# Optimization experiments

Measured on AMD Instinct MI355X. Metric: run time of the kernel, lower is better.

The kernel has to match this reference:

```python
import jax, jax.numpy as jnp
import numpy as np
from functools import partial

BATCH, SEQ = 2, 2048
D_MODEL, D_INNER, D_XB = 2048, 4096, 1024
HEADDIM, D_STATE = 64, 64
NHEADS = D_INNER // HEADDIM      # 64
NKV = D_XB // HEADDIM            # 16
REP = NHEADS // NKV              # 4
INTER = 8192
EPS = 1e-5
D_IN_PROJ = D_INNER + D_XB + D_XB + D_INNER + NHEADS  # z, x, B, C, dt


def setup_inputs() -> dict:
    key = jax.random.key(0)
    ks = jax.random.split(key, 8)
    g = lambda k, shape, s: (jax.random.normal(k, shape, jnp.float32) * s)
    return {
        "hidden_states": g(ks[0], (BATCH, SEQ, D_MODEL), 1.0),
        "ln_w": jnp.ones((D_MODEL,), jnp.float32),
        "ln_b": jnp.zeros((D_MODEL,), jnp.float32),
        "in_proj_w": g(ks[1], (D_IN_PROJ, D_MODEL), 0.02),
        "dt_bias": jax.random.uniform(ks[2], (NHEADS,), jnp.float32, -4.0, 0.0),
        "A_log": jnp.log(jnp.arange(1, NHEADS + 1, dtype=jnp.float32)),
        "Dp": jnp.ones((NHEADS,), jnp.float32),
        "norm_w": jnp.ones((D_INNER,), jnp.float32),
        "out_proj_w": g(ks[3], (D_MODEL, D_INNER), 0.02),
        "fc1_w": g(ks[4], (INTER, D_MODEL), 0.02),
        "fc1_b": jnp.zeros((INTER,), jnp.float32),
        "fc2_w": g(ks[5], (D_MODEL, INTER), 0.02),
        "fc2_b": jnp.zeros((D_MODEL,), jnp.float32),
    }


def _layernorm(x, w, b):
    mu = x.mean(-1, keepdims=True)
    var = ((x - mu) ** 2).mean(-1, keepdims=True)
    return (x - mu) * jax.lax.rsqrt(var + EPS) * w + b


def _ssd_scan(xh, dt, A, Bh, Ch):
    # xh: (b,l,h,p)  dt: (b,l,h)  A: (h,)  Bh,Ch: (b,l,h,n)
    dA = jnp.exp(dt * A)  # (b,l,h) discrete decay
    to_l = lambda t: jnp.moveaxis(t, 1, 0)  # time-major for scan

    def step(state, inp):
        dA_t, dt_t, x_t, B_t, C_t = inp
        state = state * dA_t[:, :, None, None] + jnp.einsum(
            "bh,bhp,bhn->bhpn", dt_t, x_t, B_t)
        y = jnp.einsum("bhpn,bhn->bhp", state, C_t)
        return state, y

    state0 = jnp.zeros((xh.shape[0], NHEADS, HEADDIM, D_STATE), xh.dtype)
    _, ys = jax.lax.scan(step, state0, (to_l(dA), to_l(dt), to_l(xh), to_l(Bh), to_l(Ch)))
    return jnp.moveaxis(ys, 0, 1)  # (b,l,h,p)


def reference(hidden_states, ln_w, ln_b, in_proj_w, dt_bias, A_log, Dp,
              norm_w, out_proj_w, fc1_w, fc1_b, fc2_w, fc2_b):
    residual = hidden_states
    h = _layernorm(hidden_states, ln_w, ln_b)

    # ---- Mamba2 branch ----
    zxbcdt = h @ in_proj_w.T  # (b,l,D_IN_PROJ)
    z, x, Bm, Cm, dt = jnp.split(
        zxbcdt, np.cumsum([D_INNER, D_XB, D_XB, D_INNER]).tolist(), axis=-1)
    b, l = h.shape[0], h.shape[1]
    dt = jax.nn.softplus(dt + dt_bias)               # (b,l,nheads)
    A = -jnp.exp(A_log)                              # (nheads,)
    # GQA-style repeat of x (values) and B (keys) from NKV to NHEADS groups
    xh = jnp.repeat(x.reshape(b, l, NKV, HEADDIM), REP, axis=2)   # (b,l,h,p)
    Bh = jnp.repeat(Bm.reshape(b, l, NKV, D_STATE), REP, axis=2)  # (b,l,h,n)
    Ch = Cm.reshape(b, l, NHEADS, D_STATE)                        # (b,l,h,n)

    y = _ssd_scan(xh, dt, A, Bh, Ch) + Dp[None, None, :, None] * xh
    yf = y.reshape(b, l, D_INNER)
    # gated RMSNorm (norm_before_gate=False): gate first, then rmsnorm
    yf = yf * jax.nn.silu(z)
    yf = yf * jax.lax.rsqrt((yf * yf).mean(-1, keepdims=True) + EPS) * norm_w
    mamba_out = yf @ out_proj_w.T

    # ---- Phi MLP branch (parallel, shares the layernormed input) ----
    mlp = jax.nn.gelu(h @ fc1_w.T + fc1_b, approximate=True) @ fc2_w.T + fc2_b

    # resid_dropout is identity in eval mode
    return mamba_out + mlp + residual
```

## Files before the change

kernel.cpp:

```cpp
#include <hip/hip_runtime.h>
#include <hip/hip_bf16.h>

#define BATCH 2
#define SEQ   2048
#define DMODEL 2048
#define DINNER 4096
#define DXB   1024
#define NHEADS 64
#define NKV   16
#define HEADDIM 64
#define DSTATE 64
#define INTER 8192
#define DINPROJ 10304
#define ROWS  (BATCH*SEQ)
#define NC    32
#define EPSV  1e-5f
#define TSTR  72

typedef short short8 __attribute__((ext_vector_type(8)));
typedef float f32x4 __attribute__((ext_vector_type(4)));

typedef const __attribute__((address_space(1))) unsigned int cg_u32;
typedef __attribute__((address_space(3))) unsigned int ls_u32;

static __device__ __forceinline__ void gll16(const void* g, void* l) {
    __builtin_amdgcn_global_load_lds((cg_u32*)g, (ls_u32*)l, 16, 0, 0);
}

static __device__ __forceinline__ unsigned short f2bf(float f) {
    unsigned int u = __float_as_uint(f);
    unsigned int r = (u + 0x7fffu + ((u >> 16) & 1u)) >> 16;
    return (unsigned short)r;
}
static __device__ __forceinline__ float bf2f(unsigned short h) {
    return __uint_as_float(((unsigned int)h) << 16);
}

__global__ __launch_bounds__(256) void conv4(const float* __restrict__ s0, unsigned short* __restrict__ d0, int n0,
                                             const float* __restrict__ s1, unsigned short* __restrict__ d1, int n1,
                                             const float* __restrict__ s2, unsigned short* __restrict__ d2, int n2,
                                             const float* __restrict__ s3, unsigned short* __restrict__ d3, int n3) {
    int gtid = blockIdx.x * 256 + threadIdx.x;
    int gstr = gridDim.x * 256;
    #define CSEG(S, D, N)                                         \
    for (int i = gtid; i < (N); i += gstr) {                      \
        float4 v = ((const float4*)(S))[i];                       \
        ushort4 o;                                                \
        o.x = f2bf(v.x); o.y = f2bf(v.y);                         \
        o.z = f2bf(v.z); o.w = f2bf(v.w);                         \
        ((ushort4*)(D))[i] = o;                                   \
    }
    CSEG(s0, d0, n0)
    CSEG(s1, d1, n1)
    CSEG(s2, d2, n2)
    CSEG(s3, d3, n3)
    #undef CSEG
}

__global__ __launch_bounds__(256) void ln_kernel(const float* __restrict__ x,
                                                 const float* __restrict__ w,
                                                 const float* __restrict__ b,
                                                 unsigned short* __restrict__ hout) {
    int row = blockIdx.x;
    int t = threadIdx.x;
    const float* xr = x + (size_t)row * DMODEL;
    float v[8];
    float4 v0 = *(const float4*)&xr[t * 8];
    float4 v1 = *(const float4*)&xr[t * 8 + 4];
    v[0]=v0.x; v[1]=v0.y; v[2]=v0.z; v[3]=v0.w; v[4]=v1.x; v[5]=v1.y; v[6]=v1.z; v[7]=v1.w;
    float s = 0.f, s2 = 0.f;
    #pragma unroll
    for (int i = 0; i < 8; ++i) { s += v[i]; s2 += v[i]*v[i]; }
    #pragma unroll
    for (int off = 1; off < 64; off <<= 1) { s += __shfl_xor(s, off); s2 += __shfl_xor(s2, off); }
    __shared__ float sa[4], sb[4];
    int lane = t & 63, wv = t >> 6;
    if (lane == 0) { sa[wv] = s; sb[wv] = s2; }
    __syncthreads();
    s = sa[0]+sa[1]+sa[2]+sa[3];
    s2 = sb[0]+sb[1]+sb[2]+sb[3];
    float mu = s / DMODEL;
    float var = s2 / DMODEL - mu * mu;
    float sc = rsqrtf(var + EPSV);
    unsigned short* ho = hout + (size_t)row * DMODEL + t * 8;
    #pragma unroll
    for (int i = 0; i < 8; ++i) {
        int d = t * 8 + i;
        ho[i] = f2bf((v[i] - mu) * sc * w[d] + b[d]);
    }
}

#define SLOTSZ 49152
template <int EPI>
__global__ __launch_bounds__(512, 2) void gemm_p(
    const unsigned short* __restrict__ A, const unsigned short* __restrict__ B,
    int M, int N, int K, int nby,
    float* __restrict__ outF, unsigned short* __restrict__ outH,
    const float* __restrict__ bias, const float* __restrict__ add1,
    const float* __restrict__ add2,
    const unsigned short* __restrict__ A2, const unsigned short* __restrict__ B2,
    int K1) {
    __shared__ __align__(16) char smem[3 * SLOTSZ];
    int t = threadIdx.x, lane = t & 63, w = t >> 6;
    int nwg = gridDim.x, cpx = nwg >> 3;
    int logical = (blockIdx.x & 7) * cpx + (blockIdx.x >> 3);
    int by = logical % nby, bx = logical / nby;
    int brow = by * 128, bcol = bx * 256;
    int wr = w >> 2, wc = w & 3;
    int wrb = wr * 64, wcb = wc * 64;

    int lr8 = lane >> 3;
    int lch = ((lane & 7) ^ lr8) << 3;
    const unsigned short* pa[2];
    #pragma unroll
    for (int j = 0; j < 2; ++j)
        pa[j] = A + (size_t)(brow + w * 16 + j * 8 + lr8) * K1 + lch;
    const unsigned short* pb[4];
    #pragma unroll
    for (int j = 0; j < 4; ++j) {
        int r = bcol + w * 32 + j * 8 + lr8;
        if (r > N - 1) r = N - 1;
        pb[j] = B + (size_t)r * K1 + lch;
    }
    auto stageA = [&](int slot, int j) {
        gll16(pa[j], smem + slot * SLOTSZ + (w * 16 + j * 8) * 128);
        pa[j] += 64;
    };
    auto stageB = [&](int slot, int j) {
        gll16(pb[j], smem + slot * SLOTSZ + 16384 + (w * 32 + j * 8) * 128);
        pb[j] += 64;
    };

    int arow = lane & 15;
    int swz0 = (((lane >> 4) ^ (lane & 7)) << 4);

    f32x4 acc[4][4] = {};
    const int NT = K >> 6;
    const int KS = K1 >> 6;
    #pragma unroll
    for (int j = 0; j < 2; ++j) stageA(0, j);
    #pragma unroll
    for (int j = 0; j < 4; ++j) stageB(0, j);
    #pragma unroll
    for (int j = 0; j < 2; ++j) stageA(1, j);
    #pragma unroll
    for (int j = 0; j < 4; ++j) stageB(1, j);

    int slot = 0, slot2 = 2;
    for (int kt = 0; kt < NT; ++kt) {
        if (kt + 1 < NT) { asm volatile("s_waitcnt vmcnt(6)" ::: "memory"); }
        else             { asm volatile("s_waitcnt vmcnt(0)" ::: "memory"); }
        __builtin_amdgcn_s_barrier();
        asm volatile("" ::: "memory");
        const char* Ab = smem + slot * SLOTSZ;
        const char* Bb = Ab + 16384;
        bool st = (kt + 2 < NT);
        if (B2 != nullptr && kt + 2 == KS) {
            int ld2 = K - K1;
            #pragma unroll
            for (int j = 0; j < 2; ++j)
                pa[j] = A2 + (size_t)(brow + w * 16 + j * 8 + lr8) * ld2 + lch;
            #pragma unroll
            for (int j = 0; j < 4; ++j) {
                int r = bcol + w * 32 + j * 8 + lr8;
                if (r > N - 1) r = N - 1;
                pb[j] = B2 + (size_t)r * ld2 + lch;
            }
        }
        short8 af[4], bfv[4];
        #pragma unroll
        for (int f = 0; f < 4; ++f)
            af[f] = *(const short8*)(Ab + (wrb + f * 16 + arow) * 128 + swz0);
        #pragma unroll
        for (int n = 0; n < 4; ++n)
            bfv[n] = *(const short8*)(Bb + (wcb + n * 16 + arow) * 128 + swz0);
        if (st) { stageA(slot2, 0); stageA(slot2, 1); stageB(slot2, 0); }
        __builtin_amdgcn_s_setprio(1);
        #pragma unroll
        for (int f = 0; f < 4; ++f)
            #pragma unroll
            for (int n = 0; n < 4; ++n)
                acc[f][n] = __builtin_amdgcn_mfma_f32_16x16x32_bf16(af[f], bfv[n], acc[f][n], 0, 0, 0);
        __builtin_amdgcn_s_setprio(0);
        #pragma unroll
        for (int f = 0; f < 4; ++f)
            af[f] = *(const short8*)(Ab + (wrb + f * 16 + arow) * 128 + (swz0 ^ 64));
        #pragma unroll
        for (int n = 0; n < 4; ++n)
            bfv[n] = *(const short8*)(Bb + (wcb + n * 16 + arow) * 128 + (swz0 ^ 64));
        if (st) { stageB(slot2, 1); stageB(slot2, 2); stageB(slot2, 3); }
        __builtin_amdgcn_s_setprio(1);
        #pragma unroll
        for (int f = 0; f < 4; ++f)
            #pragma unroll
            for (int n = 0; n < 4; ++n)
                acc[f][n] = __builtin_amdgcn_mfma_f32_16x16x32_bf16(af[f], bfv[n], acc[f][n], 0, 0, 0);
        __builtin_amdgcn_s_setprio(0);
        slot  = (slot  == 2) ? 0 : slot + 1;
        slot2 = (slot2 == 2) ? 0 : slot2 + 1;
    }

    int rlane = (lane >> 4) << 2, clane = lane & 15;
    #pragma unroll
    for (int f = 0; f < 4; ++f) {
        #pragma unroll
        for (int n = 0; n < 4; ++n) {
            int col = bcol + wcb + n * 16 + clane;
            if (col < N) {
                #pragma unroll
                for (int j = 0; j < 4; ++j) {
                    int row = brow + wrb + f * 16 + rlane + j;
                    size_t idx = (size_t)row * N + col;
                    float v = acc[f][n][j];
                    if constexpr (EPI == 0) {
                        outF[idx] = v;
                    } else if constexpr (EPI == 1) {
                        v += bias[col];
                        float g = 0.5f * v * (1.f + tanhf(0.7978845608f * (v + 0.044715f * v * v * v)));
                        outH[idx] = f2bf(g);
                    } else if constexpr (EPI == 2) {
                        outF[idx] = v + bias[col] + add1[idx] + add2[idx];
                    } else if constexpr (EPI == 4) {
                        outF[idx] = v + bias[col] + add2[idx];
                    } else {
                        outH[idx] = f2bf(v);
                    }
                }
            }
        }
    }
}

static __device__ __forceinline__ void mm64(const unsigned short* Al, const unsigned short* Bl,
                                            f32x4* acc, int w, int lane) {
    int lr = lane & 15, kg = (lane >> 4) << 3;
    #pragma unroll
    for (int ks = 0; ks < 2; ++ks) {
        short8 a = *(const short8*)&Al[(w * 16 + lr) * TSTR + ks * 32 + kg];
        #pragma unroll
        for (int fn = 0; fn < 4; ++fn) {
            short8 bb = *(const short8*)&Bl[(fn * 16 + lr) * TSTR + ks * 32 + kg];
            acc[fn] = __builtin_amdgcn_mfma_f32_16x16x32_bf16(a, bb, acc[fn], 0, 0, 0);
        }
    }
}

__global__ __launch_bounds__(256) void chunk_front(const unsigned short* __restrict__ zx,
                                                   const float* __restrict__ dt_bias,
                                                   const float* __restrict__ A_log,
                                                   float* __restrict__ pcum,
                                                   unsigned short* __restrict__ ybuf,
                                                   unsigned short* __restrict__ Sbuf) {
    __shared__ __align__(16) unsigned short Cs[64*TSTR], Bsr[64*TSTR], Btr[64*TSTR],
                                            Xtr[64*TSTR], Xw[64*TSTR], Wsm[64*TSTR];
    __shared__ float dts[64], clg[64];
    int t = threadIdx.x, lane = t & 63, w = t >> 6;
    int bid = blockIdx.x;
    int c = bid & 31, h = (bid >> 5) & 63, b = bid >> 11, g = h >> 2;
    int row0 = (b << 11) + (c << 6);

    if (t < 64) {
        float raw = bf2f(zx[(size_t)(row0 + t) * DINPROJ + 10240 + h]) + dt_bias[h];
        float dt = raw > 20.f ? raw : log1pf(expf(raw));
        dts[t] = dt;
        float v = dt * (-expf(A_log[h]));
        #pragma unroll
        for (int off = 1; off < 64; off <<= 1) {
            float o = __shfl_up(v, off);
            if (lane >= off) v += o;
        }
        clg[t] = v;
        pcum[(size_t)(row0 + t) * 64 + h] = expf(v);
    }
    ushort4 xr[4];
    #pragma unroll
    for (int i = 0; i < 4; ++i) {
        int q = i * 256 + t, s = q >> 4, d4 = (q & 15) << 2;
        const unsigned short* rp = zx + (size_t)(row0 + s) * DINPROJ;
        ushort4 cv = *(const ushort4*)&rp[6144 + h * 64 + d4];
        *(ushort4*)&Cs[s * TSTR + d4] = cv;
        ushort4 bv = *(const ushort4*)&rp[5120 + g * 64 + d4];
        *(ushort4*)&Bsr[s * TSTR + d4] = bv;
        Btr[(d4 + 0) * TSTR + s] = bv.x; Btr[(d4 + 1) * TSTR + s] = bv.y;
        Btr[(d4 + 2) * TSTR + s] = bv.z; Btr[(d4 + 3) * TSTR + s] = bv.w;
        ushort4 xv = *(const ushort4*)&rp[4096 + g * 64 + d4];
        Xtr[(d4 + 0) * TSTR + s] = xv.x; Xtr[(d4 + 1) * TSTR + s] = xv.y;
        Xtr[(d4 + 2) * TSTR + s] = xv.z; Xtr[(d4 + 3) * TSTR + s] = xv.w;
        xr[i] = xv;
    }
    __syncthreads();
    float cl63 = clg[63];
    #pragma unroll
    for (int i = 0; i < 4; ++i) {
        int q = i * 256 + t, s = q >> 4, d4 = (q & 15) << 2;
        float ws = dts[s] * expf(cl63 - clg[s]);
        Xw[(d4 + 0) * TSTR + s] = f2bf(bf2f(xr[i].x) * ws);
        Xw[(d4 + 1) * TSTR + s] = f2bf(bf2f(xr[i].y) * ws);
        Xw[(d4 + 2) * TSTR + s] = f2bf(bf2f(xr[i].z) * ws);
        Xw[(d4 + 3) * TSTR + s] = f2bf(bf2f(xr[i].w) * ws);
    }
    __syncthreads();
    f32x4 accG[4] = {};
    mm64(Cs, Bsr, accG, w, lane);
    int rl = (lane >> 4) << 2, cl = lane & 15;
    #pragma unroll
    for (int fn = 0; fn < 4; ++fn) {
        #pragma unroll
        for (int j = 0; j < 4; ++j) {
            int tr = w * 16 + rl + j, rc = fn * 16 + cl;
            float val = 0.f;
            if (rc <= tr) val = accG[fn][j] * expf(clg[tr] - clg[rc]) * dts[rc];
            Wsm[tr * TSTR + rc] = f2bf(val);
        }
    }
    __syncthreads();
    f32x4 accY[4] = {};
    mm64(Wsm, Xtr, accY, w, lane);
    f32x4 accS[4] = {};
    mm64(Xw, Btr, accS, w, lane);
    size_t cb = (size_t)((((b << 6) + h) << 5) + c) * 4096;
    #pragma unroll
    for (int fn = 0; fn < 4; ++fn) {
        #pragma unroll
        for (int j = 0; j < 4; ++j) {
            int tr = w * 16 + rl + j, pc = fn * 16 + cl;
            ybuf[(size_t)(row0 + tr) * DINNER + h * 64 + pc] = f2bf(accY[fn][j]);
            Sbuf[cb + tr * 64 + pc] = f2bf(accS[fn][j]);
        }
    }
}

__global__ __launch_bounds__(256) void chunk_state(unsigned short* __restrict__ SH,
                                                   const float* __restrict__ pcum) {
    int bid = blockIdx.x;
    int q = bid & 3, bh = bid >> 2;
    int b = bh >> 6, h = bh & 63;
    int t = threadIdx.x;
    float H[4];
    #pragma unroll
    for (int j = 0; j < 4; ++j) H[j] = 0.f;
    for (int c = 0; c < NC; ++c) {
        size_t base = (size_t)((((b << 6) + h) << 5) + c) * 4096 + q * 1024;
        float Tc = pcum[(size_t)((b << 11) + (c << 6) + 63) * 64 + h];
        #pragma unroll
        for (int j = 0; j < 4; ++j) {
            int e = j * 256 + t;
            unsigned short sv = SH[base + e];
            SH[base + e] = f2bf(H[j]);
            H[j] = H[j] * Tc + bf2f(sv);
        }
    }
}

__global__ __launch_bounds__(256) void chunk_back(const unsigned short* __restrict__ zx,
                                                  const unsigned short* __restrict__ SH,
                                                  const float* __restrict__ pcum,
                                                  const float* __restrict__ Dp,
                                                  unsigned short* __restrict__ ybuf) {
    __shared__ __align__(16) unsigned short Cs[64*TSTR], Hs[64*TSTR];
    __shared__ float ps[64];
    int t = threadIdx.x, lane = t & 63, w = t >> 6;
    int bid = blockIdx.x;
    int c = bid & 31, h = (bid >> 5) & 63, b = bid >> 11, g = h >> 2;
    int row0 = (b << 11) + (c << 6);
    size_t cb = (size_t)((((b << 6) + h) << 5) + c) * 4096;
    #pragma unroll
    for (int i = 0; i < 4; ++i) {
        int q = i * 256 + t, s = q >> 4, d4 = (q & 15) << 2;
        *(ushort4*)&Cs[s * TSTR + d4] =
            *(const ushort4*)&zx[(size_t)(row0 + s) * DINPROJ + 6144 + h * 64 + d4];
        *(ushort4*)&Hs[s * TSTR + d4] = *(const ushort4*)&SH[cb + s * 64 + d4];
    }
    if (t < 64) ps[t] = pcum[(size_t)(row0 + t) * 64 + h];
    __syncthreads();
    f32x4 acc[4] = {};
    mm64(Cs, Hs, acc, w, lane);
    float Dph = Dp[h];
    int rl = (lane >> 4) << 2, cl = lane & 15;
    #pragma unroll
    for (int fn = 0; fn < 4; ++fn) {
        #pragma unroll
        for (int j = 0; j < 4; ++j) {
            int tr = w * 16 + rl + j, pc = fn * 16 + cl;
            size_t yi = (size_t)(row0 + tr) * DINNER + h * 64 + pc;
            float xv = bf2f(zx[(size_t)(row0 + tr) * DINPROJ + 4096 + g * 64 + pc]);
            ybuf[yi] = f2bf(bf2f(ybuf[yi]) + acc[fn][j] * ps[tr] + Dph * xv);
        }
    }
}

__global__ __launch_bounds__(256) void gate_kernel(const unsigned short* __restrict__ y,
                                                   const unsigned short* __restrict__ zx,
                                                   const float* __restrict__ norm_w,
                                                   unsigned short* __restrict__ yf) {
    int row = blockIdx.x;
    int t = threadIdx.x;
    float v[16];
    float s2 = 0.f;
    #pragma unroll
    for (int i = 0; i < 16; ++i) {
        int d = i * 256 + t;
        float yv = bf2f(y[(size_t)row * DINNER + d]);
        float zv = bf2f(zx[(size_t)row * DINPROJ + d]);
        float gt = zv / (1.f + expf(-zv));
        v[i] = yv * gt;
        s2 += v[i] * v[i];
    }
    #pragma unroll
    for (int off = 1; off < 64; off <<= 1) s2 += __shfl_xor(s2, off);
    __shared__ float sb[4];
    int lane = t & 63, wv = t >> 6;
    if (lane == 0) sb[wv] = s2;
    __syncthreads();
    s2 = sb[0] + sb[1] + sb[2] + sb[3];
    float sc = rsqrtf(s2 / DINNER + EPSV);
    #pragma unroll
    for (int i = 0; i < 16; ++i) {
        int d = i * 256 + t;
        yf[(size_t)row * DINNER + d] = f2bf(v[i] * sc * norm_w[d]);
    }
}

extern "C" void kernel_launch(void* const* d_in, const int* in_sizes, int n_in,
                              void* d_out, int out_size, void* d_ws, size_t ws_size,
                              hipStream_t stream) {
    const float* hid   = (const float*)d_in[0];
    const float* ln_w  = (const float*)d_in[1];
    const float* ln_b  = (const float*)d_in[2];
    const float* w_inp = (const float*)d_in[3];
    const float* dtb   = (const float*)d_in[4];
    const float* A_log = (const float*)d_in[5];
    const float* Dp    = (const float*)d_in[6];
    const float* nw    = (const float*)d_in[7];
    const float* w_out = (const float*)d_in[8];
    const float* w_fc1 = (const float*)d_in[9];
    const float* fc1_b = (const float*)d_in[10];
    const float* w_fc2 = (const float*)d_in[11];
    const float* fc2_b = (const float*)d_in[12];

    char* ws = (char*)d_ws;
    size_t off = 0;
    auto alloc = [&](size_t bytes) { size_t o = off; off += (bytes + 255) & ~(size_t)255; return o; };
    size_t o_h    = alloc((size_t)ROWS * DMODEL * 2);
    size_t o_wi   = alloc((size_t)DINPROJ * DMODEL * 2);
    size_t o_wo   = alloc((size_t)DMODEL * DINNER * 2);
    size_t o_wf1  = alloc((size_t)INTER * DMODEL * 2);
    size_t o_wf2  = alloc((size_t)DMODEL * INTER * 2);
    size_t o_zx   = alloc((size_t)ROWS * DINPROJ * 2);
    size_t o_pc   = alloc((size_t)ROWS * NHEADS * 4);
    size_t o_y    = alloc((size_t)ROWS * DINNER * 2);
    size_t o_yf   = alloc((size_t)ROWS * DINNER * 2);
    size_t o_S    = alloc((size_t)BATCH * NHEADS * NC * HEADDIM * DSTATE * 2);

    unsigned short* h_bf  = (unsigned short*)(ws + o_h);
    unsigned short* wbi   = (unsigned short*)(ws + o_wi);
    unsigned short* wbo   = (unsigned short*)(ws + o_wo);
    unsigned short* wbf1  = (unsigned short*)(ws + o_wf1);
    unsigned short* wbf2  = (unsigned short*)(ws + o_wf2);
    unsigned short* zx    = (unsigned short*)(ws + o_zx);
    float* pcum           = (float*)(ws + o_pc);
    unsigned short* ybuf  = (unsigned short*)(ws + o_y);
    unsigned short* yf    = (unsigned short*)(ws + o_yf);
    unsigned short* Sbuf  = (unsigned short*)(ws + o_S);
    unsigned short* gelu  = (unsigned short*)(ws + o_zx);
    float* outF           = (float*)d_out;

    conv4<<<2048, 256, 0, stream>>>(
        w_inp, wbi,  (DINPROJ * DMODEL) / 4,
        w_out, wbo,  (DMODEL * DINNER) / 4,
        w_fc1, wbf1, (INTER * DMODEL) / 4,
        w_fc2, wbf2, (DMODEL * INTER) / 4);
    ln_kernel<<<ROWS, 256, 0, stream>>>(hid, ln_w, ln_b, h_bf);
    gemm_p<3><<<41 * 32, 512, 0, stream>>>(
        h_bf, wbi, ROWS, DINPROJ, DMODEL, 32, nullptr, zx, nullptr, nullptr, nullptr,
        nullptr, nullptr, DMODEL);
    chunk_front<<<BATCH * NHEADS * NC, 256, 0, stream>>>(zx, dtb, A_log, pcum, ybuf, Sbuf);
    chunk_state<<<BATCH * NHEADS * 4, 256, 0, stream>>>(Sbuf, pcum);
    chunk_back<<<BATCH * NHEADS * NC, 256, 0, stream>>>(zx, Sbuf, pcum, Dp, ybuf);
    gate_kernel<<<ROWS, 256, 0, stream>>>(ybuf, zx, nw, yf);
    gemm_p<1><<<32 * 32, 512, 0, stream>>>(
        h_bf, wbf1, ROWS, INTER, DMODEL, 32, nullptr, gelu, fc1_b, nullptr, nullptr,
        nullptr, nullptr, DMODEL);
    gemm_p<4><<<8 * 32, 512, 0, stream>>>(
        yf, wbo, ROWS, DMODEL, DINNER + INTER, 32, outF, nullptr, fc2_b, nullptr, hid,
        gelu, wbf2, DINNER);
}
```

Before: 761.4 us.

## Add 256x256-tile GEMM with 4-stage pipeline for in_proj and fc1

Adds a new GEMM kernel, gemm_q, that computes 256x256 output tiles with 8 waves, a 4-slot LDS ring buffer of 32-wide K steps, and one workgroup per CU. The in_proj and fc1 GEMMs now use it instead of the 128-row gemm_p. The larger tile halves the grid and raises arithmetic intensity per loaded byte, and the deeper prefetch hides global latency. The cost is higher register pressure from 32 accumulator fragments per wave and lower occupancy. Unused epilogue branches are also pruned from gemm_p.

```diff
diff --git a/kernel.cpp b/kernel.cpp
--- a/kernel.cpp
+++ b/kernel.cpp
@@ -87,6 +87,110 @@
     for (int i = 0; i < 8; ++i) {
         int d = t * 8 + i;
         ho[i] = f2bf((v[i] - mu) * sc * w[d] + b[d]);
+    }
+}
+
+#define QSLOT 32768
+template <int EPI>
+__global__ __launch_bounds__(512, 1) void gemm_q(
+    const unsigned short* __restrict__ A, const unsigned short* __restrict__ B,
+    int M, int N, int K, int nby,
+    float* __restrict__ outF, unsigned short* __restrict__ outH,
+    const float* __restrict__ bias) {
+    __shared__ __align__(16) char smem[4 * QSLOT];
+    int t = threadIdx.x, lane = t & 63, w = t >> 6;
+    int nwg = gridDim.x, cpx = nwg >> 3;
+    int logical = (blockIdx.x & 7) * cpx + (blockIdx.x >> 3);
+    int by = logical % nby, bx = logical / nby;
+    int brow = by * 256, bcol = bx * 256;
+    int wm = w >> 2, wn = w & 3;
+    int wrb = wm * 128, wcb = wn * 64;
+
+    int lrow4 = lane >> 2;
+    int scs = ((lane & 3) ^ ((lane >> 3) & 3)) << 3;
+    const unsigned short* pa[2];
+    #pragma unroll
+    for (int j = 0; j < 2; ++j)
+        pa[j] = A + (size_t)(brow + w * 32 + j * 16 + lrow4) * K + scs;
+    const unsigned short* pb[2];
+    #pragma unroll
+    for (int j = 0; j < 2; ++j) {
+        int r = bcol + w * 32 + j * 16 + lrow4;
+        if (r > N - 1) r = N - 1;
+        pb[j] = B + (size_t)r * K + scs;
+    }
+    auto stage = [&](int kt) {
+        int slot = kt & 3;
+        #pragma unroll
+        for (int j = 0; j < 2; ++j) {
+            gll16(pa[j], smem + slot * QSLOT + (w * 32 + j * 16) * 64);
+            pa[j] += 32;
+        }
+        #pragma unroll
+        for (int j = 0; j < 2; ++j) {
+            gll16(pb[j], smem + slot * QSLOT + 16384 + (w * 32 + j * 16) * 64);
+            pb[j] += 32;
+        }
+    };
+
+    int arow = lane & 15;
+    int rsw = ((lane >> 4) ^ ((arow >> 1) & 3)) << 4;
+
+    f32x4 acc[8][4] = {};
+    const int NT = K >> 5;
+    stage(0); stage(1); stage(2);
+
+    for (int kt = 0; kt < NT; ++kt) {
+        if (kt + 2 < NT)      { asm volatile("s_waitcnt vmcnt(8)" ::: "memory"); }
+        else if (kt + 1 < NT) { asm volatile("s_waitcnt vmcnt(4)" ::: "memory"); }
+        else                  { asm volatile("s_waitcnt vmcnt(0)" ::: "memory"); }
+        __builtin_amdgcn_s_barrier();
+        asm volatile("" ::: "memory");
+        const char* Ab = smem + (kt & 3) * QSLOT;
+        const char* Bb = Ab + 16384;
+        short8 af[8], bfv[4];
+        #pragma unroll
+        for (int f = 0; f < 8; ++f) {
+            int r = wrb + f * 16 + arow;
+            af[f] = *(const short8*)(Ab + r * 64 + rsw);
+        }
+        #pragma unroll
+        for (int n = 0; n < 4; ++n) {
+            int r = wcb + n * 16 + arow;
+            bfv[n] = *(const short8*)(Bb + r * 64 + rsw);
+        }
+        if (kt + 3 < NT) stage(kt + 3);
+        __builtin_amdgcn_s_setprio(1);
+        #pragma unroll
+        for (int f = 0; f < 8; ++f)
+            #pragma unroll
+            for (int n = 0; n < 4; ++n)
+                acc[f][n] = __builtin_amdgcn_mfma_f32_16x16x32_bf16(af[f], bfv[n], acc[f][n], 0, 0, 0);
+        __builtin_amdgcn_s_setprio(0);
+    }
+
+    int rlane = (lane >> 4) << 2, clane = lane & 15;
+    #pragma unroll
+    for (int f = 0; f < 8; ++f) {
+        #pragma unroll
+        for (int n = 0; n < 4; ++n) {
+            int col = bcol + wcb + n * 16 + clane;
+            if (col < N) {
+                #pragma unroll
+                for (int j = 0; j < 4; ++j) {
+                    int row = brow + wrb + f * 16 + rlane + j;
+                    size_t idx = (size_t)row * N + col;
+                    float v = acc[f][n][j];
+                    if constexpr (EPI == 1) {
+                        v += bias[col];
+                        float g = 0.5f * v * (1.f + tanhf(0.7978845608f * (v + 0.044715f * v * v * v)));
+                        outH[idx] = f2bf(g);
+                    } else {
+                        outH[idx] = f2bf(v);
+                    }
+                }
+            }
+        }
     }
 }
 
@@ -212,18 +316,10 @@
                     int row = brow + wrb + f * 16 + rlane + j;
                     size_t idx = (size_t)row * N + col;
                     float v = acc[f][n][j];
-                    if constexpr (EPI == 0) {
-                        outF[idx] = v;
-                    } else if constexpr (EPI == 1) {
-                        v += bias[col];
-                        float g = 0.5f * v * (1.f + tanhf(0.7978845608f * (v + 0.044715f * v * v * v)));
-                        outH[idx] = f2bf(g);
-                    } else if constexpr (EPI == 2) {
-                        outF[idx] = v + bias[col] + add1[idx] + add2[idx];
-                    } else if constexpr (EPI == 4) {
+                    if constexpr (EPI == 4) {
                         outF[idx] = v + bias[col] + add2[idx];
                     } else {
-                        outH[idx] = f2bf(v);
+                        outF[idx] = v;
                     }
                 }
             }
@@ -471,16 +567,14 @@
         w_fc1, wbf1, (INTER * DMODEL) / 4,
         w_fc2, wbf2, (DMODEL * INTER) / 4);
     ln_kernel<<<ROWS, 256, 0, stream>>>(hid, ln_w, ln_b, h_bf);
-    gemm_p<3><<<41 * 32, 512, 0, stream>>>(
-        h_bf, wbi, ROWS, DINPROJ, DMODEL, 32, nullptr, zx, nullptr, nullptr, nullptr,
-        nullptr, nullptr, DMODEL);
+    gemm_q<3><<<41 * 16, 512, 0, stream>>>(
+        h_bf, wbi, ROWS, DINPROJ, DMODEL, 16, nullptr, zx, nullptr);
     chunk_front<<<BATCH * NHEADS * NC, 256, 0, stream>>>(zx, dtb, A_log, pcum, ybuf, Sbuf);
     chunk_state<<<BATCH * NHEADS * 4, 256, 0, stream>>>(Sbuf, pcum);
     chunk_back<<<BATCH * NHEADS * NC, 256, 0, stream>>>(zx, Sbuf, pcum, Dp, ybuf);
     gate_kernel<<<ROWS, 256, 0, stream>>>(ybuf, zx, nw, yf);
-    gemm_p<1><<<32 * 32, 512, 0, stream>>>(
-        h_bf, wbf1, ROWS, INTER, DMODEL, 32, nullptr, gelu, fc1_b, nullptr, nullptr,
-        nullptr, nullptr, DMODEL);
+    gemm_q<1><<<32 * 16, 512, 0, stream>>>(
+        h_bf, wbf1, ROWS, INTER, DMODEL, 16, nullptr, gelu, fc1_b);
     gemm_p<4><<<8 * 32, 512, 0, stream>>>(
         yf, wbo, ROWS, DMODEL, DINNER + INTER, 32, outF, nullptr, fc2_b, nullptr, hid,
         gelu, wbf2, DINNER);
```

Measured after the change: 749.2 us (median of 2 runs). About the same (-1.6%).
